# Optimization experiments

Hardware: AMD Instinct MI355X
Metric: run time of the kernel (lower is better)

## Reference

```python
import jax, jax.numpy as jnp
import numpy as np

B, T, F = 32, 1024, 64
H = 128          # num_lstm_out
KH = 16          # kan_hidden_dim
C1, C2, C3 = 128, 256, 128
NC = 10


def _glorot(key, shape):
    fan_in = shape[0] if len(shape) == 2 else int(np.prod(shape[1:]))
    return (jax.random.normal(key, shape, jnp.float32) / np.sqrt(fan_in)).astype(jnp.float32)


def setup_inputs() -> dict:
    key = jax.random.key(0)
    ks = jax.random.split(key, 24)
    D = F + H
    d = {}
    d['x'] = jax.random.normal(ks[0], (B, T, F), jnp.float32)
    d['eps_z'] = jax.random.normal(ks[1], (B, H), jnp.float32)
    d['eps_cat'] = jax.random.normal(ks[2], (B, H), jnp.float32)
    # KAN-LSTM cell: gates = W2 @ silu(W1 @ [x;h])
    d['kan_w1'] = _glorot(ks[3], (D, KH)); d['kan_b1'] = jnp.zeros((KH,), jnp.float32)
    d['kan_w2'] = _glorot(ks[4], (KH, 4 * H)); d['kan_b2'] = jnp.zeros((4 * H,), jnp.float32)
    # causal convs (OIH layout)
    d['conv1_w'] = _glorot(ks[5], (C1, F, 8)); d['conv1_b'] = jnp.zeros((C1,), jnp.float32)
    d['conv2_w'] = _glorot(ks[6], (C2, C1, 5)); d['conv2_b'] = jnp.zeros((C2,), jnp.float32)
    d['conv3_w'] = _glorot(ks[7], (C3, C2, 3)); d['conv3_b'] = jnp.zeros((C3,), jnp.float32)
    # batchnorm affine params
    d['bn1_g'] = jnp.ones((C1,), jnp.float32); d['bn1_b'] = jnp.zeros((C1,), jnp.float32)
    d['bn2_g'] = jnp.ones((C2,), jnp.float32); d['bn2_b'] = jnp.zeros((C2,), jnp.float32)
    d['bn3_g'] = jnp.ones((C3,), jnp.float32); d['bn3_b'] = jnp.zeros((C3,), jnp.float32)
    # SE layers (reduction=16, no bias)
    d['se1_w1'] = _glorot(ks[8], (C1, C1 // 16)); d['se1_w2'] = _glorot(ks[9], (C1 // 16, C1))
    d['se2_w1'] = _glorot(ks[10], (C2, C2 // 16)); d['se2_w2'] = _glorot(ks[11], (C2 // 16, C2))
    # VIB heads
    d['fc_mu_w'] = _glorot(ks[12], (H, H)); d['fc_mu_b'] = jnp.zeros((H,), jnp.float32)
    d['fc_std_w'] = _glorot(ks[13], (H, H)); d['fc_std_b'] = jnp.zeros((H,), jnp.float32)
    d['fc_mu_cat_w'] = _glorot(ks[14], (2 * H, H)); d['fc_mu_cat_b'] = jnp.zeros((H,), jnp.float32)
    d['fc_std_cat_w'] = _glorot(ks[15], (2 * H, H)); d['fc_std_cat_b'] = jnp.zeros((H,), jnp.float32)
    d['fc_w'] = _glorot(ks[16], (H + C3, NC)); d['fc_b'] = jnp.zeros((NC,), jnp.float32)
    return d


def _kan_lstm(x, w1, b1, w2, b2):
    # x: (B,T,F) -> hidden (B,T,H); sequential recurrence via lax.scan
    xT = jnp.swapaxes(x, 0, 1)  # (T,B,F)
    h0 = jnp.zeros((x.shape[0], H), x.dtype)
    c0 = jnp.zeros((x.shape[0], H), x.dtype)

    def step(carry, xt):
        h, c = carry
        g = jax.nn.silu(jnp.concatenate([xt, h], axis=-1) @ w1 + b1) @ w2 + b2  # (B,4H)
        i_, f_, g_, o_ = jnp.split(g, 4, axis=-1)
        c = jax.nn.sigmoid(f_) * c + jax.nn.sigmoid(i_) * jnp.tanh(g_)
        h = jax.nn.sigmoid(o_) * jnp.tanh(c)
        return (h, c), h

    _, hs = jax.lax.scan(step, (h0, c0), xT)
    return jnp.swapaxes(hs, 0, 1)  # (B,T,H)


def _cluster_hidden(hidden):
    # hidden: (B,T,H). Pairwise cosine sim -> exp kernel -> best 2-block cut.
    Tn = hidden.shape[1]
    last = hidden[:, -1, :]
    hn = hidden / jnp.clip(jnp.linalg.norm(hidden, axis=-1, keepdims=True), 1e-8)
    S = jnp.exp(-5.5 * (1.0 - jnp.einsum('bik,bjk->bij', hn, hn)))  # (B,T,T)
    S = S * (1.0 - jnp.eye(Tn, dtype=S.dtype))  # zero diagonal
    # 2D prefix sums give all block sums in O(T^2) instead of O(T^3)
    P = jnp.cumsum(jnp.cumsum(S, axis=1), axis=2)
    i = jnp.arange(1, Tn)
    TL = P[:, i - 1, i - 1]                 # (B,T-1) sum of [:i,:i]
    full = P[:, -1, -1][:, None]
    TR = P[:, i - 1, -1] - TL               # sum of [:i,i:]
    BL = P[:, -1, i - 1] - TL               # sum of [i:,:i]
    BR = full - TL - TR - BL                # sum of [i:,i:]
    ii = i.astype(S.dtype)
    nn = (Tn - i).astype(S.dtype)
    dist = TL / (ii * ii) + BR / (nn * nn) - (TR + BL) / (ii * nn)
    cuts = jnp.argmax(dist, axis=1) + 1     # (B,)
    mask = (jnp.arange(Tn)[None, :] < cuts[:, None]).astype(hidden.dtype)
    corr = jnp.einsum('bt,bth->bh', mask, hidden) / cuts[:, None].astype(hidden.dtype)
    return last, corr


def _causal_conv(x, w, b):
    k = w.shape[-1]
    xp = jnp.pad(x, ((0, 0), (0, 0), (k - 1, 0)))
    y = jax.lax.conv_general_dilated(xp, w, (1,), 'VALID',
                                     dimension_numbers=('NCH', 'OIH', 'NCH'))
    return y + b[None, :, None]


def _bn(x, g, b, eps=1e-3):
    m = x.mean(axis=(0, 2), keepdims=True)
    v = x.var(axis=(0, 2), keepdims=True)
    return (x - m) / jnp.sqrt(v + eps) * g[None, :, None] + b[None, :, None]


def _se(x, w1, w2):
    y = x.mean(axis=2)                       # (B,C)
    y = jax.nn.sigmoid(jax.nn.relu(y @ w1) @ w2)
    return x * y[:, :, None]


def reference(x, eps_z, eps_cat, kan_w1, kan_b1, kan_w2, kan_b2,
              conv1_w, conv1_b, conv2_w, conv2_b, conv3_w, conv3_b,
              bn1_g, bn1_b, bn2_g, bn2_b, bn3_g, bn3_b,
              se1_w1, se1_w2, se2_w1, se2_w2,
              fc_mu_w, fc_mu_b, fc_std_w, fc_std_b,
              fc_mu_cat_w, fc_mu_cat_b, fc_std_cat_w, fc_std_cat_b,
              fc_w, fc_b):
    # LSTM branch
    hidden = _kan_lstm(x, kan_w1, kan_b1, kan_w2, kan_b2)      # (B,T,H)
    out, corr = _cluster_hidden(hidden)
    mu = corr @ fc_mu_w + fc_mu_b
    std = jax.nn.softplus(corr @ fc_std_w + fc_std_b)
    z = mu + std * eps_z
    xz = jnp.concatenate([out, z], axis=1)                      # (B,2H)
    mu_cat = xz @ fc_mu_cat_w + fc_mu_cat_b
    std_cat = jax.nn.softplus(xz @ fc_std_cat_w + fc_std_cat_b)
    x1 = mu_cat + std_cat * eps_cat   # dropout in eval mode = identity
    # FCN branch
    x2 = jnp.swapaxes(x, 1, 2)                                  # (B,F,T)
    x2 = jax.nn.gelu(_bn(_causal_conv(x2, conv1_w, conv1_b), bn1_g, bn1_b), approximate=False)
    x2 = _se(x2, se1_w1, se1_w2)
    x2 = jax.nn.gelu(_bn(_causal_conv(x2, conv2_w, conv2_b), bn2_g, bn2_b), approximate=False)
    x2 = _se(x2, se2_w1, se2_w2)
    x2 = jax.nn.gelu(_bn(_causal_conv(x2, conv3_w, conv3_b), bn3_g, bn3_b), approximate=False)
    x2 = x2.mean(axis=2)                                        # (B,C3)
    x_all = jnp.concatenate([x1, x2], axis=1)
    logits = x_all @ fc_w + fc_b
    return (jax.nn.log_softmax(logits, axis=1), mu, std, mu_cat, std_cat)
```

## Files before the change

### kernel.cpp

```cpp
#include <hip/hip_runtime.h>
#include <math.h>

#define B_ 32
#define T_ 1024
#define F_ 64
#define H_ 128
#define D_ 192
#define KH_ 16
#define C1_ 128
#define C2_ 256
#define C3_ 128
#define NC_ 10

typedef float v2f __attribute__((ext_vector_type(2)));
typedef float f32x4 __attribute__((ext_vector_type(4)));
typedef __bf16 bfrag __attribute__((ext_vector_type(8)));

__device__ __forceinline__ float sig_(float x){ return 1.f/(1.f+__expf(-x)); }
__device__ __forceinline__ float tanh_(float x){ return 1.f - 2.f/(__expf(2.f*x)+1.f); }
__device__ __forceinline__ float gelu_(float x){ return 0.5f*x*(1.f+erff(x*0.70710678118654752f)); }
__device__ __forceinline__ float softplus_(float x){ return fmaxf(x,0.f) + log1pf(__expf(-fabsf(x))); }

__device__ __forceinline__ unsigned bfpack(float a, float b){
  unsigned ua = __float_as_uint(a), ub = __float_as_uint(b);
  ua = ua + 0x7FFFu + ((ua>>16)&1u);
  ub = ub + 0x7FFFu + ((ub>>16)&1u);
  return (ua>>16) | (ub & 0xFFFF0000u);
}
__device__ __forceinline__ unsigned short bf1(float a){
  unsigned ua = __float_as_uint(a);
  ua = ua + 0x7FFFu + ((ua>>16)&1u);
  return (unsigned short)(ua>>16);
}
__device__ __forceinline__ float bf2f(unsigned short h){
  return __uint_as_float(((unsigned)h)<<16);
}

#define QPERM_XOR1(x) __int_as_float(__builtin_amdgcn_mov_dpp(__float_as_int(x), 0xB1, 0xF, 0xF, true))
#define QPERM_XOR2(x) __int_as_float(__builtin_amdgcn_mov_dpp(__float_as_int(x), 0x4E, 0xF, 0xF, true))

#define LDS_BARRIER() asm volatile("s_waitcnt lgkmcnt(0)\n\ts_barrier" ::: "memory")


__device__ __forceinline__ void ax_body(int blk, char* smemraw,
    const float* __restrict__ x, const float* __restrict__ w1, const float* __restrict__ b1,
    float* __restrict__ axT)
{
  struct AxS { float xs[16][68]; float w1s[64][16]; };
  AxS* sm = (AxS*)smemraw;
  const int bt0 = blk*16;
  const int tid = threadIdx.x;
  for(int i=tid;i<64*16;i+=256){ sm->w1s[i>>4][i&15] = w1[i]; }
  for(int i=tid;i<16*64;i+=256){ const int r=i>>6, d=i&63; sm->xs[r][d] = x[(size_t)(bt0+r)*64 + d]; }
  __syncthreads();
  const int r = tid>>4, j = tid&15;
  float s = b1[j];
  #pragma unroll
  for(int d=0; d<64; d++) s += sm->xs[r][d]*sm->w1s[d][j];
  const int bt = bt0 + r;
  axT[((size_t)(bt>>10)*16 + j)*1024 + (bt&1023)] = s;
}

__device__ __forceinline__ void prepack_body(int blk,
    const float* __restrict__ w1s, const float* __restrict__ w2s, const float* __restrict__ w3s,
    unsigned short* __restrict__ wp1, unsigned short* __restrict__ wp2, unsigned short* __restrict__ wp3)
{
  int e = blk*256 + threadIdx.x;
  if(e >= 65536+163840+98304) return;
  const float* w; unsigned short* wp; int Cout, Cin, Kw;
  if(e < 65536){ w=w1s; wp=wp1; Cout=C1_; Cin=F_;  Kw=8; }
  else if(e < 65536+163840){ e-=65536; w=w2s; wp=wp2; Cout=C2_; Cin=C1_; Kw=5; }
  else { e-=229376; w=w3s; wp=wp3; Cout=C3_; Cin=C2_; Kw=3; }
  const int co = e/(Cin*Kw);
  const int rem = e - co*(Cin*Kw);
  const int ci = rem/Kw, kw = rem - ci*Kw;
  const int off = (((ci>>5)*Kw + kw)*(Cout>>4) + (co>>4))*512 + ((co&15)*4 + ((ci>>3)&3))*8 + (ci&7);
  wp[off] = bf1(w[e]);
}

__device__ __forceinline__ void norm_body(int blk,
    const float* __restrict__ hidden,
    unsigned short* __restrict__ hnhi, unsigned short* __restrict__ hnlo)
{
  const int row = blk*8 + (threadIdx.x>>5);
  const int l = threadIdx.x&31;
  const float* hr = hidden + (size_t)row*H_;
  float s = 0.f;
  for(int k=l;k<H_;k+=32){ float v=hr[k]; s+=v*v; }
  #pragma unroll
  for(int m=16;m>=1;m>>=1) s += __shfl_xor(s, m, 64);
  const float inv = 1.f/fmaxf(sqrtf(s), 1e-8f);
  const float4 v = *(const float4*)&hr[l*4];
  const float f0=v.x*inv, f1=v.y*inv, f2=v.z*inv, f3=v.w*inv;
  const unsigned short h0=bf1(f0), h1=bf1(f1), h2=bf1(f2), h3=bf1(f3);
  uint2 phi; phi.x = (unsigned)h0 | ((unsigned)h1<<16); phi.y = (unsigned)h2 | ((unsigned)h3<<16);
  *(uint2*)&hnhi[(size_t)row*H_ + l*4] = phi;
  const unsigned short g0=bf1(f0-bf2f(h0)), g1=bf1(f1-bf2f(h1)), g2=bf1(f2-bf2f(h2)), g3=bf1(f3-bf2f(h3));
  uint2 plo; plo.x = (unsigned)g0 | ((unsigned)g1<<16); plo.y = (unsigned)g2 | ((unsigned)g3<<16);
  *(uint2*)&hnlo[(size_t)row*H_ + l*4] = plo;
}

struct SS {
  unsigned short Ahi[64*136];
  unsigned short Alo[64*136];
  unsigned short Bhi[64*136];
  unsigned short Blo[64*136];
  double red[64][17];
};
__device__ __forceinline__ void s_body(int blk, char* smemraw,
    const unsigned short* __restrict__ hnhi, const unsigned short* __restrict__ hnlo,
    double* __restrict__ rowsum, double* __restrict__ psum)
{
  SS* sm = (SS*)smemraw;
  const int b = blk >> 4;
  const int i0 = (blk & 15) * 64;
  const int tid = threadIdx.x, l = tid & 63, wv = tid >> 6;
  const int m = l & 15, q = l >> 4;

  {
    const uint4* ghi = (const uint4*)(hnhi + ((size_t)b*T_ + i0)*H_);
    const uint4* glo = (const uint4*)(hnlo + ((size_t)b*T_ + i0)*H_);
    for(int idx=tid; idx<64*16; idx+=256){
      const int r = idx>>4, c8 = idx&15;
      *(uint4*)&sm->Ahi[r*136 + c8*8] = ghi[r*16 + c8];
      *(uint4*)&sm->Alo[r*136 + c8*8] = glo[r*16 + c8];
    }
  }

  double rs[4]={0,0,0,0}, ps[4]={0,0,0,0};
  const int arow = (wv*16 + m)*136;

  for(int jt=0;jt<16;jt++){
    const int j0 = jt*64;
    __syncthreads();
    {
      const uint4* ghi = (const uint4*)(hnhi + ((size_t)b*T_ + j0)*H_);
      const uint4* glo = (const uint4*)(hnlo + ((size_t)b*T_ + j0)*H_);
      for(int idx=tid; idx<64*16; idx+=256){
        const int r = idx>>4, c8 = idx&15;
        *(uint4*)&sm->Bhi[r*136 + c8*8] = ghi[r*16 + c8];
        *(uint4*)&sm->Blo[r*136 + c8*8] = glo[r*16 + c8];
      }
    }
    __syncthreads();

    f32x4 acc[4];
    #pragma unroll
    for(int nt=0;nt<4;nt++) acc[nt] = (f32x4)(0.f);
    #pragma unroll
    for(int kc=0;kc<4;kc++){
      const bfrag Ah = *(const bfrag*)&sm->Ahi[arow + kc*32 + q*8];
      const bfrag Al = *(const bfrag*)&sm->Alo[arow + kc*32 + q*8];
      #pragma unroll
      for(int nt=0;nt<4;nt++){
        const int brow = (nt*16 + m)*136 + kc*32 + q*8;
        const bfrag Bh = *(const bfrag*)&sm->Bhi[brow];
        const bfrag Bl = *(const bfrag*)&sm->Blo[brow];
        acc[nt] = __builtin_amdgcn_mfma_f32_16x16x32_bf16(Ah, Bh, acc[nt], 0, 0, 0);
        acc[nt] = __builtin_amdgcn_mfma_f32_16x16x32_bf16(Al, Bh, acc[nt], 0, 0, 0);
        acc[nt] = __builtin_amdgcn_mfma_f32_16x16x32_bf16(Ah, Bl, acc[nt], 0, 0, 0);
      }
    }
    #pragma unroll
    for(int nt=0;nt<4;nt++){
      const int gj = j0 + nt*16 + m;
      #pragma unroll
      for(int r=0;r<4;r++){
        const int gi = i0 + wv*16 + q*4 + r;
        if(gi == gj) continue;
        const float sv = __expf(-5.5f*(1.f - acc[nt][r]));
        rs[r] += (double)sv;
        if(gj < gi) ps[r] += (double)sv;
      }
    }
  }
  __syncthreads();
  #pragma unroll
  for(int r=0;r<4;r++) sm->red[wv*16 + q*4 + r][m] = rs[r];
  __syncthreads();
  if(tid<64){ double v=0; for(int k=0;k<16;k++) v+=sm->red[tid][k]; rowsum[(size_t)b*T_ + i0 + tid]=v; }
  __syncthreads();
  #pragma unroll
  for(int r=0;r<4;r++) sm->red[wv*16 + q*4 + r][m] = ps[r];
  __syncthreads();
  if(tid<64){ double v=0; for(int k=0;k<16;k++) v+=sm->red[tid][k]; psum[(size_t)b*T_ + i0 + tid]=v; }
}

struct CS {
  double sr[256]; double sp[256]; double bd[256]; double totR;
  float c2[2][128]; int bidx[256]; int cut;
};
__device__ __forceinline__ void cluster_body(int b, char* smemraw,
    const double* __restrict__ rowsum, const double* __restrict__ psum,
    const float* __restrict__ hidden, float* __restrict__ corr, int* __restrict__ cuts)
{
  CS* sm = (CS*)smemraw;
  const int tid = threadIdx.x;
  const double* r = rowsum + (size_t)b*T_;
  const double* p = psum + (size_t)b*T_;
  double r4[4], p4[4];
  #pragma unroll
  for(int q=0;q<4;q++){ r4[q]=r[tid*4+q]; p4[q]=p[tid*4+q]; }
  sm->sr[tid]=r4[0]+r4[1]+r4[2]+r4[3];
  sm->sp[tid]=p4[0]+p4[1]+p4[2]+p4[3];
  __syncthreads();
  if(tid==0){
    double ar=0, ap=0;
    for(int i=0;i<256;i++){ double tr=sm->sr[i], tp=sm->sp[i]; sm->sr[i]=ar; sm->sp[i]=ap; ar+=tr; ap+=tp; }
    sm->totR = ar;
  }
  __syncthreads();
  double cr = sm->sr[tid], cp = sm->sp[tid];
  const double full = sm->totR;
  double best = -1e308; int bi = 1;
  #pragma unroll
  for(int q=0;q<4;q++){
    cr += r4[q]; cp += p4[q];
    const int i = 4*tid + q + 1;
    if(i < T_){
      const double TL = 2.0*cp;
      const double TRv = cr - TL;
      const double BR = full - TL - 2.0*TRv;
      const double di = (double)i, dn = (double)(T_-i);
      const double dist = TL/(di*di) + BR/(dn*dn) - (2.0*TRv)/(di*dn);
      if(dist > best){ best=dist; bi=i; }
    }
  }
  sm->bd[tid]=best; sm->bidx[tid]=bi;
  __syncthreads();
  if(tid==0){
    double bb=-1e308; int ii=1;
    for(int q=0;q<256;q++){ if(sm->bd[q]>bb){ bb=sm->bd[q]; ii=sm->bidx[q]; } }
    sm->cut=ii; cuts[b]=ii;
  }
  __syncthreads();
  const int cut = sm->cut;
  const int h = tid&127, half = tid>>7;
  float s=0.f;
  const float* hb = hidden + (size_t)b*T_*H_;
  #pragma unroll 4
  for(int t=half; t<cut; t+=2) s += hb[(size_t)t*H_ + h];
  sm->c2[half][h]=s;
  __syncthreads();
  if(tid<128) corr[b*H_+tid] = (sm->c2[0][tid]+sm->c2[1][tid])/(float)cut;
}

__device__ __forceinline__ void head1_body(int b, char* smemraw,
    const float* __restrict__ corr, const float* __restrict__ hidden,
    const float* __restrict__ eps_z, const float* __restrict__ eps_cat,
    const float* __restrict__ mu_w, const float* __restrict__ mu_b,
    const float* __restrict__ std_w, const float* __restrict__ std_b,
    const float* __restrict__ muc_w, const float* __restrict__ muc_b,
    const float* __restrict__ stdc_w, const float* __restrict__ stdc_b,
    float* __restrict__ out_mu, float* __restrict__ out_std,
    float* __restrict__ out_muc, float* __restrict__ out_stdc, float* __restrict__ x1)
{
  struct H1 { float cs[128]; float xz[256]; };
  H1* sm = (H1*)smemraw;
  const int h = threadIdx.x;
  if(h<128){
    sm->cs[h]=corr[b*H_+h];
    sm->xz[h]=hidden[((size_t)b*T_ + (T_-1))*H_ + h];
  }
  __syncthreads();
  if(h<128){
    float m=mu_b[h], sdv=std_b[h];
    for(int k=0;k<H_;k++){ const float cv=sm->cs[k]; m+=cv*mu_w[k*H_+h]; sdv+=cv*std_w[k*H_+h]; }
    const float stdv = softplus_(sdv);
    out_mu[b*H_+h]=m; out_std[b*H_+h]=stdv;
    sm->xz[128+h] = m + stdv*eps_z[b*H_+h];
  }
  __syncthreads();
  if(h<128){
    float mc=muc_b[h], sc=stdc_b[h];
    for(int k=0;k<256;k++){ const float v=sm->xz[k]; mc+=v*muc_w[k*H_+h]; sc+=v*stdc_w[k*H_+h]; }
    const float stdc = softplus_(sc);
    out_muc[b*H_+h]=mc; out_stdc[b*H_+h]=stdc;
    x1[b*H_+h]=mc + stdc*eps_cat[b*H_+h];
  }
}

struct ConvS {
  float sescale[256];
  float seh[16];
  unsigned short xs[72*40];
};
__device__ __forceinline__ void conv_body(int bx, int by, int bz, char* smemraw,
    const float* __restrict__ in, const unsigned short* __restrict__ wp,
    const float* __restrict__ bias,
    const float* __restrict__ se_in, const float* __restrict__ se_w1,
    const float* __restrict__ se_w2, int seR,
    float* __restrict__ y, float* __restrict__ bnacc, int Cin, int Cout, int Kw)
{
  ConvS* sm = (ConvS*)smemraw;
  unsigned short* xs = sm->xs;
  const int b = bz, t0 = bx*64, co0 = by*64;
  const int tid = threadIdx.x, l = tid&63, wv = tid>>6;
  const int q = l>>4, m = l&15;
  const int TW = 64 + Kw - 1;
  const int abase = (wv*16 + m)*40 + q*8;
  const int boff = (m*4 + q)*8;
  const bool use_se = (se_in != nullptr);

  if(use_se){
    float* ms = (float*)xs;
    if(tid<Cin) ms[tid] = se_in[b*Cin+tid] * (1.f/(float)T_);
    __syncthreads();
    if(tid<seR){ float s=0.f; for(int k=0;k<Cin;k++) s += ms[k]*se_w1[k*seR+tid]; sm->seh[tid]=fmaxf(s,0.f); }
    __syncthreads();
    if(tid<Cin){ float s=0.f; for(int k=0;k<seR;k++) s += sm->seh[k]*se_w2[k*Cin+tid]; sm->sescale[tid]=sig_(s); }
  }

  f32x4 acc[4];
  #pragma unroll
  for(int nt=0;nt<4;nt++) acc[nt] = (f32x4)(0.f);

  const int nchunks = Cin >> 5;
  for(int cc=0; cc<nchunks; cc++){
    __syncthreads();
    for(int idx=tid; idx<TW*8; idx+=256){
      const int r = idx>>3, c4 = (idx&7)*4;
      const int tg = t0 - (Kw-1) + r;
      uint2 pk = make_uint2(0u, 0u);
      if(tg >= 0){
        float4 v = *(const float4*)&in[((size_t)b*T_ + tg)*Cin + cc*32 + c4];
        if(use_se){
          const float4 s4 = *(const float4*)&sm->sescale[cc*32 + c4];
          v.x*=s4.x; v.y*=s4.y; v.z*=s4.z; v.w*=s4.w;
        }
        pk.x = bfpack(v.x, v.y); pk.y = bfpack(v.z, v.w);
      }
      *(uint2*)&xs[r*40 + c4] = pk;
    }
    __syncthreads();
    for(int kw=0; kw<Kw; kw++){
      const bfrag Af = *(const bfrag*)&xs[abase + kw*40];
      #pragma unroll
      for(int nt=0; nt<4; nt++){
        const unsigned short* wpp = wp + ((size_t)((cc*Kw + kw)*(Cout>>4) + (by*4 + nt)))*512 + boff;
        const bfrag Bf = *(const bfrag*)wpp;
        acc[nt] = __builtin_amdgcn_mfma_f32_16x16x32_bf16(Af, Bf, acc[nt], 0, 0, 0);
      }
    }
  }
  __syncthreads();
  float* part = (float*)xs;
  const int t_base = t0 + wv*16 + q*4;
  #pragma unroll
  for(int nt=0; nt<4; nt++){
    const int co = co0 + nt*16 + m;
    const float bv = bias[co];
    float s1 = 0.f, s2 = 0.f;
    #pragma unroll
    for(int r=0;r<4;r++){
      const float v = acc[nt][r] + bv;
      y[((size_t)b*T_ + t_base + r)*Cout + co] = v;
      s1 += v; s2 += v*v;
    }
    s1 += __shfl_xor(s1, 16); s1 += __shfl_xor(s1, 32);
    s2 += __shfl_xor(s2, 16); s2 += __shfl_xor(s2, 32);
    if(q==0){ part[(wv*64 + nt*16 + m)*2+0] = s1; part[(wv*64 + nt*16 + m)*2+1] = s2; }
  }
  __syncthreads();
  if(tid < 64){
    float a1=0.f, a2=0.f;
    #pragma unroll
    for(int w2i=0; w2i<4; w2i++){ a1 += part[(w2i*64+tid)*2+0]; a2 += part[(w2i*64+tid)*2+1]; }
    atomicAdd(&bnacc[co0 + tid], a1);
    atomicAdd(&bnacc[Cout + co0 + tid], a2);
  }
}

__device__ __forceinline__ void bn_act_body(int b, int chunk, char* smemraw,
    float* __restrict__ y, const float* __restrict__ bnacc,
    const float* __restrict__ gw, const float* __restrict__ bw,
    float* __restrict__ mean_acc, int C, int write_y)
{
  const int t0 = chunk*128, tid = threadIdx.x;
  const int c = tid & (C-1), part = tid / C, np = 256 / C;
  const float cnt = (float)(B_*T_);
  const float mm = bnacc[c]/cnt;
  const float var = bnacc[C+c]/cnt - mm*mm;
  const float sc = gw[c]/sqrtf(var+1e-3f);
  const float sh = bw[c] - mm*sc;
  float s = 0.f;
  for(int t=t0+part; t<t0+128; t+=np){
    const size_t off = ((size_t)b*T_ + t)*C + c;
    float v = y[off];
    v = gelu_(v*sc + sh);
    if(write_y) y[off] = v;
    s += v;
  }
  float* rs = (float*)smemraw;
  if(np > 1){
    rs[tid]=s;
    __syncthreads();
    if(part==0) s += rs[tid+C];
  }
  if(part==0) atomicAdd(&mean_acc[b*C+c], s);
}

__device__ __forceinline__ void lstm_body(int b, char* smemraw,
    const float* __restrict__ axT, const float* __restrict__ w1,
    const float* __restrict__ w2, const float* __restrict__ b2,
    float* __restrict__ hidden)
{
  float (*hs)[148] = (float(*)[148])smemraw;
  const int tid = threadIdx.x;
  const int l = tid & 63, wv = tid >> 6;
  const int j = l >> 2, g = l & 3;
  const int hi = wv*64 + l;

  v2f w1hv[16];
  #pragma unroll
  for(int q=0;q<16;q++){
    w1hv[q].x = w1[(64 + g*32 + 2*q)*KH_ + j];
    w1hv[q].y = w1[(64 + g*32 + 2*q + 1)*KH_ + j];
  }
  v2f w2if[16], w2go[16];
  #pragma unroll
  for(int k=0;k<16;k++){
    w2if[k].x = w2[k*512 + hi];       w2if[k].y = w2[k*512 + 128 + hi];
    w2go[k].x = w2[k*512 + 256 + hi]; w2go[k].y = w2[k*512 + 384 + hi];
  }
  v2f bif, bgo;
  bif.x = b2[hi]; bif.y = b2[128+hi]; bgo.x = b2[256+hi]; bgo.y = b2[384+hi];

  for(int i=tid;i<2*148;i+=128) ((float*)hs)[i]=0.f;
  float c = 0.f;
  const float* axr = axT + ((size_t)b*16 + j)*1024;
  float* hb = hidden + (size_t)b*T_*H_;
  const int hwi = (hi>>5)*36 + (hi&31);
  float4 axA = *(const float4*)&axr[0];
  float4 axB = *(const float4*)&axr[4];
  __syncthreads();

#define LSTM_STEP(tt, axv, RB) { \
    const float* hsr = hs[RB]; \
    float* hsw = hs[1-(RB)]; \
    v2f ap0=(v2f)(0.f), ap1=(v2f)(0.f), ap2=(v2f)(0.f), ap3=(v2f)(0.f); \
    { const float4 hv = *(const float4*)&hsr[g*36 + 0];  ap0 += ((v2f){hv.x,hv.y})*w1hv[0]  + ((v2f){hv.z,hv.w})*w1hv[1]; } \
    { const float4 hv = *(const float4*)&hsr[g*36 + 4];  ap1 += ((v2f){hv.x,hv.y})*w1hv[2]  + ((v2f){hv.z,hv.w})*w1hv[3]; } \
    { const float4 hv = *(const float4*)&hsr[g*36 + 8];  ap2 += ((v2f){hv.x,hv.y})*w1hv[4]  + ((v2f){hv.z,hv.w})*w1hv[5]; } \
    { const float4 hv = *(const float4*)&hsr[g*36 + 12]; ap3 += ((v2f){hv.x,hv.y})*w1hv[6]  + ((v2f){hv.z,hv.w})*w1hv[7]; } \
    { const float4 hv = *(const float4*)&hsr[g*36 + 16]; ap0 += ((v2f){hv.x,hv.y})*w1hv[8]  + ((v2f){hv.z,hv.w})*w1hv[9]; } \
    { const float4 hv = *(const float4*)&hsr[g*36 + 20]; ap1 += ((v2f){hv.x,hv.y})*w1hv[10] + ((v2f){hv.z,hv.w})*w1hv[11]; } \
    { const float4 hv = *(const float4*)&hsr[g*36 + 24]; ap2 += ((v2f){hv.x,hv.y})*w1hv[12] + ((v2f){hv.z,hv.w})*w1hv[13]; } \
    { const float4 hv = *(const float4*)&hsr[g*36 + 28]; ap3 += ((v2f){hv.x,hv.y})*w1hv[14] + ((v2f){hv.z,hv.w})*w1hv[15]; } \
    const v2f apt = (ap0+ap1)+(ap2+ap3); \
    float a = apt.x + apt.y; \
    a += QPERM_XOR1(a); \
    a += QPERM_XOR2(a); \
    a += (axv); \
    const float g1 = a * sig_(a); \
    v2f aIF = bif, aGO = bgo; \
    _Pragma("unroll") \
    for(int k=0;k<16;k++){ \
      const float gk = __int_as_float(__builtin_amdgcn_readlane(__float_as_int(g1), 4*k)); \
      v2f gk2; gk2.x=gk; gk2.y=gk; \
      aIF += gk2 * w2if[k]; \
      aGO += gk2 * w2go[k]; \
    } \
    const float si = sig_(aIF.x); \
    const float sf = sig_(aIF.y); \
    const float tg = tanh_(aGO.x); \
    const float so = sig_(aGO.y); \
    c = sf*c + si*tg; \
    const float h = so * tanh_(c); \
    hsw[hwi] = h; \
    hb[(size_t)(tt)*H_ + hi] = h; \
    LDS_BARRIER(); \
  }

  for(int t0=0;t0<T_;t0+=4){
    const int tl = (t0+8 < 1020) ? (t0+8) : 1020;
    const float4 axC = *(const float4*)&axr[tl];
    LSTM_STEP(t0+0, axA.x, 0)
    LSTM_STEP(t0+1, axA.y, 1)
    LSTM_STEP(t0+2, axA.z, 0)
    LSTM_STEP(t0+3, axA.w, 1)
    axA = axB; axB = axC;
  }
#undef LSTM_STEP
}


__global__ __launch_bounds__(256) void mega0_kernel(
    const float* c1w, const float* c2w, const float* c3w,
    unsigned short* wp1, unsigned short* wp2, unsigned short* wp3,
    const float* x, const float* kw1, const float* kb1, float* axT)
{
  __shared__ __align__(16) char sm[16*68*4 + 64*16*4];
  const int bid = blockIdx.x;
  if(bid < 1280) prepack_body(bid, c1w, c2w, c3w, wp1, wp2, wp3);
  else ax_body(bid-1280, sm, x, kw1, kb1, axT);
}

__global__ __launch_bounds__(256) void fusedA_kernel(
    const float* axT, const float* kw1, const float* kw2, const float* kb2, float* hidden,
    const float* x, const unsigned short* wp1, const float* c1b, float* y1, float* bn1)
{
  __shared__ __align__(16) char sm[sizeof(ConvS)];
  const int bid = blockIdx.x;
  if(bid < 32){
    if(threadIdx.x >= 128){
      #pragma nounroll
      for(int i=0;i<1025;i++){ asm volatile("s_barrier" ::: "memory"); }
      return;
    }
    __builtin_amdgcn_s_setprio(1);
    lstm_body(bid, sm, axT, kw1, kw2, kb2, hidden);
  } else {
    const int cb = bid - 32;
    conv_body(cb&15, (cb>>4)&1, cb>>5, sm, x, wp1, c1b,
              nullptr, nullptr, nullptr, 0, y1, bn1, F_, C1_, 8);
  }
}

__global__ __launch_bounds__(256) void megaA2_kernel(
    const float* hidden, unsigned short* hnhi, unsigned short* hnlo,
    float* y1, const float* bn1, const float* g1w, const float* b1w, float* se1_in)
{
  __shared__ __align__(16) char sm[1536];
  const int bid = blockIdx.x;
  if(bid < 4096) norm_body(bid, hidden, hnhi, hnlo);
  else { const int cb = bid-4096; bn_act_body(cb>>3, cb&7, sm, y1, bn1, g1w, b1w, se1_in, C1_, 1); }
}

__global__ __launch_bounds__(256) void s_kernel(
    const unsigned short* hnhi, const unsigned short* hnlo, double* rowsum, double* psum)
{
  __shared__ __align__(16) char sm[sizeof(SS)];
  s_body(blockIdx.x, sm, hnhi, hnlo, rowsum, psum);
}

__global__ __launch_bounds__(256) void megaC_kernel(
    const double* rowsum, const double* psum, const float* hidden, float* corr, int* cuts,
    const float* y1, const unsigned short* wp2, const float* c2b,
    const float* se1_in, const float* s1w1, const float* s1w2,
    float* y2, float* bn2)
{
  __shared__ __align__(16) char sm[sizeof(CS) > sizeof(ConvS) ? sizeof(CS) : sizeof(ConvS)];
  const int bid = blockIdx.x;
  if(bid < 32) cluster_body(bid, sm, rowsum, psum, hidden, corr, cuts);
  else {
    const int cb = bid - 32;
    conv_body(cb&15, (cb>>4)&3, cb>>6, sm, y1, wp2, c2b,
              se1_in, s1w1, s1w2, C1_/16, y2, bn2, C1_, C2_, 5);
  }
}

__global__ __launch_bounds__(256) void megaD_kernel(
    const float* corr, const float* hidden, const float* eps_z, const float* eps_cat,
    const float* mu_w, const float* mu_b, const float* std_w, const float* std_b,
    const float* muc_w, const float* muc_b, const float* stdc_w, const float* stdc_b,
    float* out_mu, float* out_std, float* out_muc, float* out_stdc, float* x1,
    float* y2, const float* bn2, const float* g2w, const float* b2w, float* se2_in)
{
  __shared__ __align__(16) char sm[1536];
  const int bid = blockIdx.x;
  if(bid < 32) head1_body(bid, sm, corr, hidden, eps_z, eps_cat, mu_w, mu_b, std_w, std_b,
                          muc_w, muc_b, stdc_w, stdc_b, out_mu, out_std, out_muc, out_stdc, x1);
  else { const int cb = bid-32; bn_act_body(cb>>3, cb&7, sm, y2, bn2, g2w, b2w, se2_in, C2_, 1); }
}

__global__ __launch_bounds__(256) void conv3_kernel(
    const float* y2, const unsigned short* wp3, const float* c3b,
    const float* se2_in, const float* s2w1, const float* s2w2,
    float* y3, float* bn3)
{
  __shared__ __align__(16) char sm[sizeof(ConvS)];
  const int bid = blockIdx.x;
  conv_body(bid&15, (bid>>4)&1, bid>>5, sm, y2, wp3, c3b,
            se2_in, s2w1, s2w2, C2_/16, y3, bn3, C2_, C3_, 3);
}

__global__ __launch_bounds__(256) void bn3_kernel(
    float* y3, const float* bn3, const float* g3w, const float* b3w, float* x2)
{
  __shared__ __align__(16) char sm[1024];
  const int bid = blockIdx.x;
  bn_act_body(bid>>3, bid&7, sm, y3, bn3, g3w, b3w, x2, C3_, 0);
}

__global__ __launch_bounds__(64) void head2_kernel(
    const float* __restrict__ x1, const float* __restrict__ x2,
    const float* __restrict__ fcw, const float* __restrict__ fcb, float* __restrict__ outls)
{
  const int b=blockIdx.x, tid=threadIdx.x;
  __shared__ float xa[256]; __shared__ float lg[NC_];
  for(int k=tid;k<256;k+=64) xa[k] = (k<128)? x1[b*128+k] : x2[b*128+(k-128)]*(1.f/(float)T_);
  __syncthreads();
  if(tid<NC_){
    float s = fcb[tid];
    for(int k=0;k<256;k++) s += xa[k]*fcw[k*NC_+tid];
    lg[tid]=s;
  }
  __syncthreads();
  if(tid==0){
    float mx=lg[0];
    for(int q=1;q<NC_;q++) mx=fmaxf(mx,lg[q]);
    float se=0;
    for(int q=0;q<NC_;q++) se += __expf(lg[q]-mx);
    const float lse = logf(se)+mx;
    for(int q=0;q<NC_;q++) outls[b*NC_+q] = lg[q]-lse;
  }
}

extern "C" void kernel_launch(void* const* d_in, const int* in_sizes, int n_in,
                              void* d_out, int out_size, void* d_ws, size_t ws_size,
                              hipStream_t stream) {
  (void)in_sizes; (void)n_in; (void)out_size; (void)ws_size;
  const float* x        = (const float*)d_in[0];
  const float* eps_z    = (const float*)d_in[1];
  const float* eps_cat  = (const float*)d_in[2];
  const float* kan_w1   = (const float*)d_in[3];
  const float* kan_b1   = (const float*)d_in[4];
  const float* kan_w2   = (const float*)d_in[5];
  const float* kan_b2   = (const float*)d_in[6];
  const float* conv1_w  = (const float*)d_in[7];
  const float* conv1_b  = (const float*)d_in[8];
  const float* conv2_w  = (const float*)d_in[9];
  const float* conv2_b  = (const float*)d_in[10];
  const float* conv3_w  = (const float*)d_in[11];
  const float* conv3_b  = (const float*)d_in[12];
  const float* bn1_g    = (const float*)d_in[13];
  const float* bn1_b    = (const float*)d_in[14];
  const float* bn2_g    = (const float*)d_in[15];
  const float* bn2_b    = (const float*)d_in[16];
  const float* bn3_g    = (const float*)d_in[17];
  const float* bn3_b    = (const float*)d_in[18];
  const float* se1_w1   = (const float*)d_in[19];
  const float* se1_w2   = (const float*)d_in[20];
  const float* se2_w1   = (const float*)d_in[21];
  const float* se2_w2   = (const float*)d_in[22];
  const float* fc_mu_w  = (const float*)d_in[23];
  const float* fc_mu_b  = (const float*)d_in[24];
  const float* fc_std_w = (const float*)d_in[25];
  const float* fc_std_b = (const float*)d_in[26];
  const float* fc_muc_w = (const float*)d_in[27];
  const float* fc_muc_b = (const float*)d_in[28];
  const float* fc_stdc_w= (const float*)d_in[29];
  const float* fc_stdc_b= (const float*)d_in[30];
  const float* fc_w     = (const float*)d_in[31];
  const float* fc_b     = (const float*)d_in[32];

  float* out = (float*)d_out;
  float* out_ls   = out;
  float* out_mu   = out + 320;
  float* out_std  = out + 320 + 4096;
  float* out_muc  = out + 320 + 2*4096;
  float* out_stdc = out + 320 + 3*4096;

  float* ws = (float*)d_ws;
  const size_t SZ_HID = (size_t)B_*T_*H_;
  const size_t SZ_Y1  = (size_t)B_*T_*C1_;
  const size_t SZ_Y2  = (size_t)B_*T_*C2_;
  float*  hidden = ws;
  float*  y1     = hidden + SZ_HID;
  float*  y2     = y1 + SZ_Y1;
  double* rowsum = (double*)(y2 + SZ_Y2);
  double* psum   = rowsum + (size_t)B_*T_;
  float*  corr   = (float*)(psum + (size_t)B_*T_);
  float*  x1     = corr + (size_t)B_*H_;
  float*  bnbuf  = x1 + (size_t)B_*H_;
  float*  bn1    = bnbuf;
  float*  bn2    = bnbuf + 2*C1_;
  float*  bn3    = bnbuf + 2*C1_ + 2*C2_;
  float*  se1_in = bnbuf + 1024;
  float*  se2_in = se1_in + (size_t)B_*C1_;
  float*  x2     = se2_in + (size_t)B_*C2_;
  int*    cuts   = (int*)(x2 + (size_t)B_*C3_);
  float*  axbuf  = (float*)(cuts + B_);
  unsigned short* wp1 = (unsigned short*)(axbuf + (size_t)B_*16*T_);
  unsigned short* wp2 = wp1 + (size_t)C1_*F_*8;
  unsigned short* wp3 = wp2 + (size_t)C2_*C1_*5;
  unsigned short* hnhi = wp3 + (size_t)C3_*C2_*3;
  unsigned short* hnlo = hnhi + (size_t)B_*T_*H_;
  float*  y3     = y1;

  hipMemsetAsync(bnbuf, 0, (size_t)(1024 + B_*C1_ + B_*C2_ + B_*C3_)*sizeof(float), stream);

  mega0_kernel<<<3328, 256, 0, stream>>>(conv1_w, conv2_w, conv3_w, wp1, wp2, wp3,
                                         x, kan_w1, kan_b1, axbuf);
  fusedA_kernel<<<32 + 1024, 256, 0, stream>>>(axbuf, kan_w1, kan_w2, kan_b2, hidden,
                                               x, wp1, conv1_b, y1, bn1);
  megaA2_kernel<<<4096 + 256, 256, 0, stream>>>(hidden, hnhi, hnlo,
                                                y1, bn1, bn1_g, bn1_b, se1_in);
  s_kernel<<<512, 256, 0, stream>>>(hnhi, hnlo, rowsum, psum);
  megaC_kernel<<<32 + 2048, 256, 0, stream>>>(rowsum, psum, hidden, corr, cuts,
                                              y1, wp2, conv2_b, se1_in, se1_w1, se1_w2, y2, bn2);
  megaD_kernel<<<32 + 256, 256, 0, stream>>>(corr, hidden, eps_z, eps_cat,
      fc_mu_w, fc_mu_b, fc_std_w, fc_std_b, fc_muc_w, fc_muc_b, fc_stdc_w, fc_stdc_b,
      out_mu, out_std, out_muc, out_stdc, x1,
      y2, bn2, bn2_g, bn2_b, se2_in);
  conv3_kernel<<<1024, 256, 0, stream>>>(y2, wp3, conv3_b, se2_in, se2_w1, se2_w2, y3, bn3);
  bn3_kernel<<<256, 256, 0, stream>>>(y3, bn3, bn3_g, bn3_b, x2);
  head2_kernel<<<B_, 64, 0, stream>>>(x1, x2, fc_w, fc_b, out_ls);
}
```

Before: 884.5 us.

## Run entire FCN branch as persistent workers alongside LSTM using grid barriers

The whole conv/BN/SE FCN branch (conv1, bn1, conv2, bn2, conv3, bn3) now runs inside the same kernel as the sequential LSTM recurrence. It uses 448 persistent worker blocks that synchronise through a software global barrier. The aim is to hide the FCN work entirely under the latency-bound LSTM blocks. The norm, cluster, head1 and head2 stages become separate, smaller kernels that start only after the LSTM finishes. This adds the risk of deadlock if the worker blocks are not all co-resident, and it makes LSTM blocks compete with the workers for compute.

```diff
diff --git a/kernel.cpp b/kernel.cpp
--- a/kernel.cpp
+++ b/kernel.cpp
@@ -11,6 +11,7 @@
 #define C2_ 256
 #define C3_ 128
 #define NC_ 10
+#define KWORK 448
 
 typedef float v2f __attribute__((ext_vector_type(2)));
 typedef float f32x4 __attribute__((ext_vector_type(4)));
@@ -40,6 +41,25 @@
 #define QPERM_XOR2(x) __int_as_float(__builtin_amdgcn_mov_dpp(__float_as_int(x), 0x4E, 0xF, 0xF, true))
 
 #define LDS_BARRIER() asm volatile("s_waitcnt lgkmcnt(0)\n\ts_barrier" ::: "memory")
+
+__device__ __forceinline__ void workerbar(int* cnt, int* gen){
+  __threadfence();
+  __syncthreads();
+  if(threadIdx.x==0){
+    const int g = __hip_atomic_load(gen, __ATOMIC_RELAXED, __HIP_MEMORY_SCOPE_AGENT);
+    const int v = __hip_atomic_fetch_add(cnt, 1, __ATOMIC_ACQ_REL, __HIP_MEMORY_SCOPE_AGENT);
+    if(v == KWORK-1){
+      __hip_atomic_store(cnt, 0, __ATOMIC_RELAXED, __HIP_MEMORY_SCOPE_AGENT);
+      __hip_atomic_fetch_add(gen, 1, __ATOMIC_RELEASE, __HIP_MEMORY_SCOPE_AGENT);
+    } else {
+      while(__hip_atomic_load(gen, __ATOMIC_ACQUIRE, __HIP_MEMORY_SCOPE_AGENT) == g){
+        __builtin_amdgcn_s_sleep(8);
+      }
+    }
+  }
+  __syncthreads();
+  __threadfence();
+}
 
 
 __device__ __forceinline__ void ax_body(int blk, char* smemraw,
@@ -369,6 +389,7 @@
     atomicAdd(&bnacc[co0 + tid], a1);
     atomicAdd(&bnacc[Cout + co0 + tid], a2);
   }
+  __syncthreads();
 }
 
 __device__ __forceinline__ void bn_act_body(int b, int chunk, char* smemraw,
@@ -396,6 +417,7 @@
     rs[tid]=s;
     __syncthreads();
     if(part==0) s += rs[tid+C];
+    __syncthreads();
   }
   if(part==0) atomicAdd(&mean_acc[b*C+c], s);
 }
@@ -496,9 +518,17 @@
   else ax_body(bid-1280, sm, x, kw1, kb1, axT);
 }
 
-__global__ __launch_bounds__(256) void fusedA_kernel(
+__global__ __launch_bounds__(256, 2) void fusedA_kernel(
     const float* axT, const float* kw1, const float* kw2, const float* kb2, float* hidden,
-    const float* x, const unsigned short* wp1, const float* c1b, float* y1, float* bn1)
+    const float* x, const unsigned short* wp1, const float* c1b, float* y1, float* bn1,
+    const float* g1w, const float* b1w, float* se1_in,
+    const unsigned short* wp2, const float* c2b, const float* s1w1, const float* s1w2,
+    float* y2, float* bn2,
+    const float* g2w, const float* b2w, float* se2_in,
+    const unsigned short* wp3, const float* c3b, const float* s2w1, const float* s2w2,
+    float* y3, float* bn3,
+    const float* g3w, const float* b3w, float* x2,
+    int* barcnt, int* bargen)
 {
   __shared__ __align__(16) char sm[sizeof(ConvS)];
   const int bid = blockIdx.x;
@@ -510,21 +540,35 @@
     }
     __builtin_amdgcn_s_setprio(1);
     lstm_body(bid, sm, axT, kw1, kw2, kb2, hidden);
-  } else {
-    const int cb = bid - 32;
-    conv_body(cb&15, (cb>>4)&1, cb>>5, sm, x, wp1, c1b,
+    return;
+  }
+  const int wid = bid - 32;
+  for(int it=wid; it<1024; it+=KWORK)
+    conv_body(it&15, (it>>4)&1, it>>5, sm, x, wp1, c1b,
               nullptr, nullptr, nullptr, 0, y1, bn1, F_, C1_, 8);
-  }
-}
-
-__global__ __launch_bounds__(256) void megaA2_kernel(
-    const float* hidden, unsigned short* hnhi, unsigned short* hnlo,
-    float* y1, const float* bn1, const float* g1w, const float* b1w, float* se1_in)
-{
-  __shared__ __align__(16) char sm[1536];
-  const int bid = blockIdx.x;
-  if(bid < 4096) norm_body(bid, hidden, hnhi, hnlo);
-  else { const int cb = bid-4096; bn_act_body(cb>>3, cb&7, sm, y1, bn1, g1w, b1w, se1_in, C1_, 1); }
+  workerbar(barcnt, bargen);
+  for(int it=wid; it<256; it+=KWORK)
+    bn_act_body(it>>3, it&7, sm, y1, bn1, g1w, b1w, se1_in, C1_, 1);
+  workerbar(barcnt, bargen);
+  for(int it=wid; it<2048; it+=KWORK)
+    conv_body(it&15, (it>>4)&3, it>>6, sm, y1, wp2, c2b,
+              se1_in, s1w1, s1w2, C1_/16, y2, bn2, C1_, C2_, 5);
+  workerbar(barcnt, bargen);
+  for(int it=wid; it<256; it+=KWORK)
+    bn_act_body(it>>3, it&7, sm, y2, bn2, g2w, b2w, se2_in, C2_, 1);
+  workerbar(barcnt, bargen);
+  for(int it=wid; it<1024; it+=KWORK)
+    conv_body(it&15, (it>>4)&1, it>>5, sm, y2, wp3, c3b,
+              se2_in, s2w1, s2w2, C2_/16, y3, bn3, C2_, C3_, 3);
+  workerbar(barcnt, bargen);
+  for(int it=wid; it<256; it+=KWORK)
+    bn_act_body(it>>3, it&7, sm, y3, bn3, g3w, b3w, x2, C3_, 0);
+}
+
+__global__ __launch_bounds__(256) void norm_kernel(
+    const float* hidden, unsigned short* hnhi, unsigned short* hnlo)
+{
+  norm_body(blockIdx.x, hidden, hnhi, hnlo);
 }
 
 __global__ __launch_bounds__(256) void s_kernel(
@@ -534,76 +578,38 @@
   s_body(blockIdx.x, sm, hnhi, hnlo, rowsum, psum);
 }
 
-__global__ __launch_bounds__(256) void megaC_kernel(
+__global__ __launch_bounds__(256) void tail_kernel(
     const double* rowsum, const double* psum, const float* hidden, float* corr, int* cuts,
-    const float* y1, const unsigned short* wp2, const float* c2b,
-    const float* se1_in, const float* s1w1, const float* s1w2,
-    float* y2, float* bn2)
-{
-  __shared__ __align__(16) char sm[sizeof(CS) > sizeof(ConvS) ? sizeof(CS) : sizeof(ConvS)];
-  const int bid = blockIdx.x;
-  if(bid < 32) cluster_body(bid, sm, rowsum, psum, hidden, corr, cuts);
-  else {
-    const int cb = bid - 32;
-    conv_body(cb&15, (cb>>4)&3, cb>>6, sm, y1, wp2, c2b,
-              se1_in, s1w1, s1w2, C1_/16, y2, bn2, C1_, C2_, 5);
-  }
-}
-
-__global__ __launch_bounds__(256) void megaD_kernel(
-    const float* corr, const float* hidden, const float* eps_z, const float* eps_cat,
+    const float* eps_z, const float* eps_cat,
     const float* mu_w, const float* mu_b, const float* std_w, const float* std_b,
     const float* muc_w, const float* muc_b, const float* stdc_w, const float* stdc_b,
     float* out_mu, float* out_std, float* out_muc, float* out_stdc, float* x1,
-    float* y2, const float* bn2, const float* g2w, const float* b2w, float* se2_in)
-{
-  __shared__ __align__(16) char sm[1536];
-  const int bid = blockIdx.x;
-  if(bid < 32) head1_body(bid, sm, corr, hidden, eps_z, eps_cat, mu_w, mu_b, std_w, std_b,
-                          muc_w, muc_b, stdc_w, stdc_b, out_mu, out_std, out_muc, out_stdc, x1);
-  else { const int cb = bid-32; bn_act_body(cb>>3, cb&7, sm, y2, bn2, g2w, b2w, se2_in, C2_, 1); }
-}
-
-__global__ __launch_bounds__(256) void conv3_kernel(
-    const float* y2, const unsigned short* wp3, const float* c3b,
-    const float* se2_in, const float* s2w1, const float* s2w2,
-    float* y3, float* bn3)
-{
-  __shared__ __align__(16) char sm[sizeof(ConvS)];
-  const int bid = blockIdx.x;
-  conv_body(bid&15, (bid>>4)&1, bid>>5, sm, y2, wp3, c3b,
-            se2_in, s2w1, s2w2, C2_/16, y3, bn3, C2_, C3_, 3);
-}
-
-__global__ __launch_bounds__(256) void bn3_kernel(
-    float* y3, const float* bn3, const float* g3w, const float* b3w, float* x2)
-{
-  __shared__ __align__(16) char sm[1024];
-  const int bid = blockIdx.x;
-  bn_act_body(bid>>3, bid&7, sm, y3, bn3, g3w, b3w, x2, C3_, 0);
-}
-
-__global__ __launch_bounds__(64) void head2_kernel(
-    const float* __restrict__ x1, const float* __restrict__ x2,
-    const float* __restrict__ fcw, const float* __restrict__ fcb, float* __restrict__ outls)
-{
-  const int b=blockIdx.x, tid=threadIdx.x;
-  __shared__ float xa[256]; __shared__ float lg[NC_];
-  for(int k=tid;k<256;k+=64) xa[k] = (k<128)? x1[b*128+k] : x2[b*128+(k-128)]*(1.f/(float)T_);
+    const float* x2, const float* fcw, const float* fcb, float* outls)
+{
+  __shared__ __align__(16) char sm[sizeof(CS)];
+  const int b = blockIdx.x, tid = threadIdx.x;
+  cluster_body(b, sm, rowsum, psum, hidden, corr, cuts);
+  __syncthreads();
+  head1_body(b, sm, corr, hidden, eps_z, eps_cat, mu_w, mu_b, std_w, std_b,
+             muc_w, muc_b, stdc_w, stdc_b, out_mu, out_std, out_muc, out_stdc, x1);
+  __syncthreads();
+  struct H2 { float xa[256]; float lg[NC_]; };
+  H2* s2 = (H2*)sm;
+  s2->xa[tid] = (tid<128) ? x1[b*128+tid] : x2[b*128+(tid-128)]*(1.f/(float)T_);
   __syncthreads();
   if(tid<NC_){
     float s = fcb[tid];
-    for(int k=0;k<256;k++) s += xa[k]*fcw[k*NC_+tid];
-    lg[tid]=s;
+    for(int k=0;k<256;k++) s += s2->xa[k]*fcw[k*NC_+tid];
+    s2->lg[tid]=s;
   }
   __syncthreads();
   if(tid==0){
-    float mx=lg[0];
-    for(int q=1;q<NC_;q++) mx=fmaxf(mx,lg[q]);
+    float mx=s2->lg[0];
+    for(int q=1;q<NC_;q++) mx=fmaxf(mx,s2->lg[q]);
     float se=0;
-    for(int q=0;q<NC_;q++) se += __expf(lg[q]-mx);
+    for(int q=0;q<NC_;q++) se += __expf(s2->lg[q]-mx);
     const float lse = logf(se)+mx;
-    for(int q=0;q<NC_;q++) outls[b*NC_+q] = lg[q]-lse;
+    for(int q=0;q<NC_;q++) outls[b*NC_+q] = s2->lg[q]-lse;
   }
 }
 
@@ -670,7 +676,8 @@
   float*  se1_in = bnbuf + 1024;
   float*  se2_in = se1_in + (size_t)B_*C1_;
   float*  x2     = se2_in + (size_t)B_*C2_;
-  int*    cuts   = (int*)(x2 + (size_t)B_*C3_);
+  int*    barv   = (int*)(x2 + (size_t)B_*C3_);
+  int*    cuts   = barv + 2;
   float*  axbuf  = (float*)(cuts + B_);
   unsigned short* wp1 = (unsigned short*)(axbuf + (size_t)B_*16*T_);
   unsigned short* wp2 = wp1 + (size_t)C1_*F_*8;
@@ -679,22 +686,24 @@
   unsigned short* hnlo = hnhi + (size_t)B_*T_*H_;
   float*  y3     = y1;
 
-  hipMemsetAsync(bnbuf, 0, (size_t)(1024 + B_*C1_ + B_*C2_ + B_*C3_)*sizeof(float), stream);
+  hipMemsetAsync(bnbuf, 0, (size_t)(1024 + B_*C1_ + B_*C2_ + B_*C3_ + 2)*sizeof(float), stream);
 
   mega0_kernel<<<3328, 256, 0, stream>>>(conv1_w, conv2_w, conv3_w, wp1, wp2, wp3,
                                          x, kan_w1, kan_b1, axbuf);
-  fusedA_kernel<<<32 + 1024, 256, 0, stream>>>(axbuf, kan_w1, kan_w2, kan_b2, hidden,
-                                               x, wp1, conv1_b, y1, bn1);
-  megaA2_kernel<<<4096 + 256, 256, 0, stream>>>(hidden, hnhi, hnlo,
-                                                y1, bn1, bn1_g, bn1_b, se1_in);
+  fusedA_kernel<<<32 + KWORK, 256, 0, stream>>>(
+      axbuf, kan_w1, kan_w2, kan_b2, hidden,
+      x, wp1, conv1_b, y1, bn1,
+      bn1_g, bn1_b, se1_in,
+      wp2, conv2_b, se1_w1, se1_w2, y2, bn2,
+      bn2_g, bn2_b, se2_in,
+      wp3, conv3_b, se2_w1, se2_w2, y3, bn3,
+      bn3_g, bn3_b, x2,
+      barv, barv+1);
+  norm_kernel<<<4096, 256, 0, stream>>>(hidden, hnhi, hnlo);
   s_kernel<<<512, 256, 0, stream>>>(hnhi, hnlo, rowsum, psum);
-  megaC_kernel<<<32 + 2048, 256, 0, stream>>>(rowsum, psum, hidden, corr, cuts,
-                                              y1, wp2, conv2_b, se1_in, se1_w1, se1_w2, y2, bn2);
-  megaD_kernel<<<32 + 256, 256, 0, stream>>>(corr, hidden, eps_z, eps_cat,
+  tail_kernel<<<B_, 256, 0, stream>>>(rowsum, psum, hidden, corr, cuts,
+      eps_z, eps_cat,
       fc_mu_w, fc_mu_b, fc_std_w, fc_std_b, fc_muc_w, fc_muc_b, fc_stdc_w, fc_stdc_b,
       out_mu, out_std, out_muc, out_stdc, x1,
-      y2, bn2, bn2_g, bn2_b, se2_in);
-  conv3_kernel<<<1024, 256, 0, stream>>>(y2, wp3, conv3_b, se2_in, se2_w1, se2_w2, y3, bn3);
-  bn3_kernel<<<256, 256, 0, stream>>>(y3, bn3, bn3_g, bn3_b, x2);
-  head2_kernel<<<B_, 64, 0, stream>>>(x1, x2, fc_w, fc_b, out_ls);
-}
+      x2, fc_w, fc_b, out_ls);
+}
```

Result: slower. 1.535 ms (+73.5%).
